# Optimization experiments

Hardware: AMD Instinct MI355X
Metric: run time of the kernel (lower is better)

Reference implementation:

```python
import jax, jax.numpy as jnp
import numpy as np

EPS = 1e-5

def _rms(x, w):
    # RMSNorm over last dim (head_dim), affine weight w
    v = jnp.mean(jnp.square(x), axis=-1, keepdims=True)
    return x * jax.lax.rsqrt(v + EPS) * w

def _rope(x, cos, sin):
    # x: [B, N, H, D]; cos/sin: [N, D] (interleaved-pair convention)
    xr = x.reshape(*x.shape[:-1], -1, 2)
    rot = jnp.stack([-xr[..., 1], xr[..., 0]], axis=-1).reshape(x.shape)
    return x * cos[None, :, None, :] + rot * sin[None, :, None, :]

def _rope_tables(n, d):
    pos = np.arange(n, dtype=np.float32)
    freqs = 1.0 / (10000.0 ** (np.arange(0, d, 2, dtype=np.float32) / d))
    ang = pos[:, None] * freqs[None, :]          # [n, d/2]
    ang = np.repeat(ang, 2, axis=1)              # [n, d] interleaved pairs
    return jnp.asarray(np.cos(ang)), jnp.asarray(np.sin(ang))

def setup_inputs() -> dict:
    key = jax.random.key(0)
    ks = jax.random.split(key, 6)
    B, N1, N2, C, H, D = 2, 1536, 512, 1024, 16, 64
    cos1, sin1 = _rope_tables(N1, D)
    cos2, sin2 = _rope_tables(N2, D)
    s = 0.02
    return dict(
        seq_len=N1,
        x=jax.random.normal(ks[0], (B, N1, C), jnp.float32),
        y=jax.random.normal(ks[1], (B, N2, C), jnp.float32),
        cos1=cos1, sin1=sin1, cos2=cos2, sin2=sin2,
        W_qkv_xs=jax.random.normal(ks[2], (3 * C, C), jnp.float32) * s,
        W_qkv_au=jax.random.normal(ks[3], (3 * C, C), jnp.float32) * s,
        xs_q_w=jnp.ones((D,), jnp.float32), xs_k_w=jnp.ones((D,), jnp.float32),
        au_q_w=jnp.ones((D,), jnp.float32), au_k_w=jnp.ones((D,), jnp.float32),
        W_xs_proj=jax.random.normal(ks[4], (C, C), jnp.float32) * s,
        b_xs_proj=jnp.zeros((C,), jnp.float32),
        W_au_proj=jax.random.normal(ks[5], (C, C), jnp.float32) * s,
        b_au_proj=jnp.zeros((C,), jnp.float32),
    )

def reference(seq_len, x, y, cos1, sin1, cos2, sin2,
              W_qkv_xs, W_qkv_au, xs_q_w, xs_k_w, au_q_w, au_k_w,
              W_xs_proj, b_xs_proj, W_au_proj, b_au_proj):
    B, N1, C = x.shape
    N2 = y.shape[1]
    D = xs_q_w.shape[0]
    H = C // D
    scale = D ** -0.5

    # visual stream: QKV -> per-head RMSNorm -> RoPE
    xq, xk, xv = jnp.split(x @ W_qkv_xs.T, 3, axis=-1)          # each [B,N1,C]
    xq = _rms(xq.reshape(B, N1, H, D), xs_q_w)
    xk = _rms(xk.reshape(B, N1, H, D), xs_k_w)
    xv = xv.reshape(B, N1, H, D).transpose(0, 2, 1, 3)           # [B,H,N1,D]
    xq = _rope(xq, cos1, sin1).transpose(0, 2, 1, 3)             # [B,H,N1,D]
    xk = _rope(xk, cos1, sin1).transpose(0, 2, 1, 3)

    # audio stream: QKV -> per-head RMSNorm -> RoPE
    aq, ak, av = jnp.split(y @ W_qkv_au.T, 3, axis=-1)
    aq = _rms(aq.reshape(B, N2, H, D), au_q_w)
    ak = _rms(ak.reshape(B, N2, H, D), au_k_w)
    av = av.reshape(B, N2, H, D).transpose(0, 2, 1, 3)           # [B,H,N2,D]
    aq = _rope(aq, cos2, sin2).transpose(0, 2, 1, 3)             # [B,H,N2,D]
    ak = _rope(ak, cos2, sin2).transpose(0, 2, 1, 3)

    # joint attention over concatenated sequence
    q = jnp.concatenate([xq, aq], axis=2)                        # [B,H,N1+N2,D]
    k = jnp.concatenate([xk, ak], axis=2)
    v = jnp.concatenate([xv, av], axis=2)
    attn = jax.nn.softmax(jnp.einsum('bhqd,bhkd->bhqk', q * scale, k), axis=-1)
    o = jnp.einsum('bhqk,bhkd->bhqd', attn, v)
    o = o.transpose(0, 2, 1, 3).reshape(B, N1 + N2, C)

    xs = o[:, :N1] @ W_xs_proj.T + b_xs_proj
    au = o[:, N1:] @ W_au_proj.T + b_au_proj
    return xs, au
```

## Files before the change

### kernel.cpp

```cpp
#include <hip/hip_runtime.h>
#include <hip/hip_bf16.h>

typedef __bf16 bf16_t;
typedef bf16_t bf16x4_t __attribute__((ext_vector_type(4)));
typedef bf16_t bf16x8_t __attribute__((ext_vector_type(8)));
typedef float f32x4_t __attribute__((ext_vector_type(4)));
typedef float f32x16_t __attribute__((ext_vector_type(16)));

constexpr int kB = 2, kN1 = 1536, kN2 = 512, kN = 2048, kC = 1024, kH = 16, kD = 64;
constexpr int BK = 64, LDT = 72;

__device__ inline uint32_t pack2bf(float a, float b) {
  union { bf16_t h[2]; uint32_t u; } t;
  t.h[0] = (bf16_t)a; t.h[1] = (bf16_t)b;
  return t.u;
}
__device__ inline void pl32_swap(uint32_t& a, uint32_t& b) {
  asm volatile("v_permlane32_swap_b32 %0, %1" : "+v"(a), "+v"(b));
}
__device__ __forceinline__ void gl16(const bf16_t* g, bf16_t* l) {
  __builtin_amdgcn_global_load_lds(
      (const __attribute__((address_space(1))) unsigned int*)g,
      (__attribute__((address_space(3))) unsigned int*)l, 16, 0, 0);
}

__global__ __launch_bounds__(256)
void cvt_bf16(const float* __restrict__ x, const float* __restrict__ y,
              const float* __restrict__ wqx, const float* __restrict__ wqa,
              const float* __restrict__ wpx, const float* __restrict__ wpa,
              bf16_t* __restrict__ Xb, bf16_t* __restrict__ Wq, bf16_t* __restrict__ Wp)
{
  const int bid = blockIdx.x;
  const float* src; bf16_t* dst; size_t off;
  if (bid < 192)      { src = x;   dst = Xb;           off = (size_t)bid * 16384; }
  else if (bid < 256) { src = y;   dst = Xb + 3145728; off = (size_t)(bid - 192) * 16384; }
  else if (bid < 448) { src = wqx; dst = Wq;           off = (size_t)(bid - 256) * 16384; }
  else if (bid < 640) { src = wqa; dst = Wq + 3145728; off = (size_t)(bid - 448) * 16384; }
  else if (bid < 704) { src = wpx; dst = Wp;           off = (size_t)(bid - 640) * 16384; }
  else                { src = wpa; dst = Wp + 1048576; off = (size_t)(bid - 704) * 16384; }
  src += off; dst += off;
  const int t = threadIdx.x;
  #pragma unroll
  for (int i = 0; i < 16; ++i) {
    const int e = (t + i * 256) * 4;
    f32x4_t v = *(const f32x4_t*)(src + e);
    bf16x4_t o;
    #pragma unroll
    for (int j = 0; j < 4; ++j) o[j] = (bf16_t)v[j];
    *(bf16x4_t*)(dst + e) = o;
  }
}

__global__ __launch_bounds__(256, 2)
void qkv_gemm(const bf16_t* __restrict__ Xb, const bf16_t* __restrict__ Wq,
              const float* __restrict__ cos1, const float* __restrict__ sin1,
              const float* __restrict__ cos2, const float* __restrict__ sin2,
              const float* __restrict__ xs_qw, const float* __restrict__ xs_kw,
              const float* __restrict__ au_qw, const float* __restrict__ au_kw,
              bf16_t* __restrict__ Qb, bf16_t* __restrict__ Kb, bf16_t* __restrict__ Vt)
{
  __shared__ __align__(16) bf16_t smem[32768];
  const int tid = threadIdx.x, lane = tid & 63, w = tid >> 6;
  const int wr = w >> 1, wc = w & 1;
  const int bm = blockIdx.x, bn = blockIdx.y;
  const int l15 = lane & 15, l4 = (lane >> 4) & 3;
  const int K = kC;
  const bool is_xs = bm < 24;

  const bf16_t* Ag = Xb + (size_t)bm * 128 * K;
  const bf16_t* Bg = Wq + (is_xs ? (size_t)0 : (size_t)3072 * 1024) + (size_t)bn * 128 * K;

  const int srow_l = lane >> 3;
  const int scc = (((lane & 7) ^ ((lane >> 3) & 7)) << 3);

  auto stage = [&](int c, int kt) {
    const int k0 = kt * BK;
    bf16_t* Ab = smem + c * 8192;
    bf16_t* Bb = smem + 16384 + c * 8192;
    #pragma unroll
    for (int i = 0; i < 4; ++i) {
      const int row = w * 32 + i * 8 + srow_l;
      gl16(Ag + (size_t)row * K + k0 + scc, Ab + (w * 32 + i * 8) * 64);
      gl16(Bg + (size_t)row * K + k0 + scc, Bb + (w * 32 + i * 8) * 64);
    }
  };

  f32x4_t acc[4][4] = {};
  const int nk = K / BK;
  stage(0, 0);
  asm volatile("s_waitcnt vmcnt(0)" ::: "memory");
  __syncthreads();

  int cur = 0;
  for (int kt = 0; kt < nk; ++kt) {
    if (kt + 1 < nk) stage(cur ^ 1, kt + 1);
    const bf16_t* Ab = smem + cur * 8192;
    const bf16_t* Bb = smem + 16384 + cur * 8192;
    #pragma unroll
    for (int kk = 0; kk < 2; ++kk) {
      bf16x8_t a[4], b[4];
      #pragma unroll
      for (int m = 0; m < 4; ++m) {
        const int row = wr * 64 + m * 16 + l15;
        const int cc = (kk * 32 + l4 * 8) ^ ((row & 7) << 3);
        a[m] = *(const bf16x8_t*)&Ab[row * 64 + cc];
      }
      #pragma unroll
      for (int n = 0; n < 4; ++n) {
        const int row = wc * 64 + n * 16 + l15;
        const int cc = (kk * 32 + l4 * 8) ^ ((row & 7) << 3);
        b[n] = *(const bf16x8_t*)&Bb[row * 64 + cc];
      }
      #pragma unroll
      for (int m = 0; m < 4; ++m)
        #pragma unroll
        for (int n = 0; n < 4; ++n)
          acc[m][n] = __builtin_amdgcn_mfma_f32_16x16x32_bf16(a[m], b[n], acc[m][n], 0, 0, 0);
    }
    asm volatile("s_waitcnt vmcnt(0)" ::: "memory");
    __syncthreads();
    cur ^= 1;
  }

  const int sec = bn >> 3;
  const int grow0 = bm * 128;
  int b, n0, seq_off; const float* cT; const float* sT;
  if (is_xs) { b = grow0 / 1536; n0 = grow0 - b * 1536; seq_off = 0; cT = cos1; sT = sin1; }
  else { const int g2 = grow0 - 3072; b = g2 >> 9; n0 = g2 & 511; seq_off = 1536; cT = cos2; sT = sin2; }
  const int h = (bn & 7) * 2 + wc;

  if (sec < 2) {
    const float* wsel = is_xs ? (sec == 0 ? xs_qw : xs_kw) : (sec == 0 ? au_qw : au_kw);
    float wv[4];
    #pragma unroll
    for (int n = 0; n < 4; ++n) wv[n] = wsel[n * 16 + l15];
    bf16_t* Out = (sec == 0 ? Qb : Kb) + (((size_t)b * kH + h) * kN + seq_off + n0) * kD;
    const float qscale = (sec == 0) ? 0.125f * 1.44269504088896f : 1.0f;
    #pragma unroll
    for (int m = 0; m < 4; ++m)
      #pragma unroll
      for (int r = 0; r < 4; ++r) {
        const int rl = wr * 64 + m * 16 + l4 * 4 + r;
        float ss = 0.0f;
        #pragma unroll
        for (int n = 0; n < 4; ++n) ss += acc[m][n][r] * acc[m][n][r];
        ss += __shfl_xor(ss, 1); ss += __shfl_xor(ss, 2);
        ss += __shfl_xor(ss, 4); ss += __shfl_xor(ss, 8);
        const float rinv = rsqrtf(ss * (1.0f / 64.0f) + 1e-5f);
        const int nrow = n0 + rl;
        #pragma unroll
        for (int n = 0; n < 4; ++n) {
          const int dd = n * 16 + l15;
          const float xn = acc[m][n][r] * rinv * wv[n];
          const float partner = __shfl_xor(xn, 1);
          if (!(l15 & 1)) {
            const float c = cT[(size_t)nrow * 64 + dd];
            const float s = sT[(size_t)nrow * 64 + dd];
            const float ve = (xn * c - partner * s) * qscale;
            const float vo = (partner * c + xn * s) * qscale;
            *(uint32_t*)&Out[(size_t)rl * kD + dd] = pack2bf(ve, vo);
          }
        }
      }
  } else {
    bf16_t* Lt = smem;
    #pragma unroll
    for (int m = 0; m < 4; ++m)
      #pragma unroll
      for (int n = 0; n < 4; ++n) {
        const int col = wc * 64 + n * 16 + l15;
        #pragma unroll
        for (int j = 0; j < 2; ++j) {
          const int row = wr * 64 + m * 16 + l4 * 4 + j * 2;
          *(uint32_t*)&Lt[col * 136 + row] = pack2bf(acc[m][n][j * 2], acc[m][n][j * 2 + 1]);
        }
      }
    __syncthreads();
    const int seg = tid >> 1, half = tid & 1;
    const int hl = seg >> 6, dd = seg & 63;
    bf16_t* Vo = Vt + (((size_t)b * kH + (bn & 7) * 2 + hl) * kD + dd) * kN
                 + seq_off + n0 + half * 64;
    #pragma unroll
    for (int jj = 0; jj < 8; ++jj)
      *(bf16x8_t*)&Vo[jj * 8] = *(const bf16x8_t*)&Lt[seg * 136 + half * 64 + jj * 8];
  }
}

__global__ __launch_bounds__(256, 2)
void proj_gemm(const bf16_t* __restrict__ Ob, const bf16_t* __restrict__ Wp,
               const float* __restrict__ bxs, const float* __restrict__ bau,
               float* __restrict__ out)
{
  __shared__ __align__(16) bf16_t smem[32768];
  const int tid = threadIdx.x, lane = tid & 63, w = tid >> 6;
  const int wr = w >> 1, wc = w & 1;
  const int bm = blockIdx.x, bn = blockIdx.y;
  const int l15 = lane & 15, l4 = (lane >> 4) & 3;
  const int K = kC, N = kC;

  const int grow = bm * 128;
  const int b = grow >> 11, n0r = grow & 2047;
  const bf16_t* Bg; const float* bias; float* Cg;
  if (n0r < kN1) { Bg = Wp; bias = bxs; Cg = out + ((size_t)b * kN1 + n0r) * kC; }
  else { Bg = Wp + (size_t)1024 * 1024; bias = bau;
         Cg = out + (size_t)kB * kN1 * kC + ((size_t)b * kN2 + (n0r - kN1)) * kC; }
  Bg += (size_t)bn * 128 * K;
  const bf16_t* Ag = Ob + (size_t)grow * K;

  const int srow_l = lane >> 3;
  const int scc = (((lane & 7) ^ ((lane >> 3) & 7)) << 3);

  auto stage = [&](int c, int kt) {
    const int k0 = kt * BK;
    bf16_t* Ab = smem + c * 8192;
    bf16_t* Bb = smem + 16384 + c * 8192;
    #pragma unroll
    for (int i = 0; i < 4; ++i) {
      const int row = w * 32 + i * 8 + srow_l;
      gl16(Ag + (size_t)row * K + k0 + scc, Ab + (w * 32 + i * 8) * 64);
      gl16(Bg + (size_t)row * K + k0 + scc, Bb + (w * 32 + i * 8) * 64);
    }
  };

  f32x4_t acc[4][4] = {};
  const int nk = K / BK;
  stage(0, 0);
  asm volatile("s_waitcnt vmcnt(0)" ::: "memory");
  __syncthreads();

  int cur = 0;
  for (int kt = 0; kt < nk; ++kt) {
    if (kt + 1 < nk) stage(cur ^ 1, kt + 1);
    const bf16_t* Ab = smem + cur * 8192;
    const bf16_t* Bb = smem + 16384 + cur * 8192;
    #pragma unroll
    for (int kk = 0; kk < 2; ++kk) {
      bf16x8_t a[4], bfr[4];
      #pragma unroll
      for (int m = 0; m < 4; ++m) {
        const int row = wr * 64 + m * 16 + l15;
        const int cc = (kk * 32 + l4 * 8) ^ ((row & 7) << 3);
        a[m] = *(const bf16x8_t*)&Ab[row * 64 + cc];
      }
      #pragma unroll
      for (int n = 0; n < 4; ++n) {
        const int row = wc * 64 + n * 16 + l15;
        const int cc = (kk * 32 + l4 * 8) ^ ((row & 7) << 3);
        bfr[n] = *(const bf16x8_t*)&Bb[row * 64 + cc];
      }
      #pragma unroll
      for (int m = 0; m < 4; ++m)
        #pragma unroll
        for (int n = 0; n < 4; ++n)
          acc[m][n] = __builtin_amdgcn_mfma_f32_16x16x32_bf16(a[m], bfr[n], acc[m][n], 0, 0, 0);
    }
    asm volatile("s_waitcnt vmcnt(0)" ::: "memory");
    __syncthreads();
    cur ^= 1;
  }

  float bv[4];
  #pragma unroll
  for (int n = 0; n < 4; ++n) bv[n] = bias[bn * 128 + wc * 64 + n * 16 + l15];
  #pragma unroll
  for (int m = 0; m < 4; ++m)
    #pragma unroll
    for (int n = 0; n < 4; ++n) {
      const int col = bn * 128 + wc * 64 + n * 16 + l15;
      #pragma unroll
      for (int r = 0; r < 4; ++r) {
        const int row = wr * 64 + m * 16 + l4 * 4 + r;
        Cg[(size_t)row * N + col] = acc[m][n][r] + bv[n];
      }
    }
}

__global__ __launch_bounds__(512, 2)
void flash_attn(const bf16_t* __restrict__ Q, const bf16_t* __restrict__ K,
                const bf16_t* __restrict__ Vt, bf16_t* __restrict__ O)
{
  __shared__ __align__(16) bf16_t smem[18432];
  const int tid = threadIdx.x, lane = tid & 63, w = tid >> 6;
  const int l31 = lane & 31, hi8 = ((lane >> 5) << 3), hi4 = ((lane >> 5) << 2);
  const int qt = blockIdx.x, h = blockIdx.y, b = blockIdx.z;
  const size_t headoff = ((size_t)(b * kH + h)) * kN * kD;
  const bf16_t* Kg = K + headoff;
  const bf16_t* Vg = Vt + headoff;

  bf16x8_t qf[4];
  {
    const bf16_t* Qg = Q + headoff + (size_t)(qt * 256 + w * 32 + l31) * kD + hi8;
    #pragma unroll
    for (int ks = 0; ks < 4; ++ks) qf[ks] = *(const bf16x8_t*)(Qg + ks * 16);
  }
  bf16x8_t onesv;
  #pragma unroll
  for (int j = 0; j < 8; ++j) onesv[j] = (bf16_t)1.0f;

  const int srow = tid >> 3, sc = (tid & 7) * 8;
  bf16x8_t kreg = *(const bf16x8_t*)(Kg + srow * kD + sc);
  bf16x8_t vreg = *(const bf16x8_t*)(Vg + (size_t)srow * kN + sc);

  f32x16_t oA0 = {}, oA1 = {}, accl = {};

  for (int kt = 0; kt < kN / 64; ++kt) {
    const int cur = kt & 1;
    bf16_t* Kc = smem + cur * 4608;
    bf16_t* Vc = smem + 9216 + cur * 4608;
    *(bf16x8_t*)&Kc[srow * LDT + sc] = kreg;
    *(bf16x8_t*)&Vc[srow * LDT + sc] = vreg;
    if (kt + 1 < kN / 64) {
      kreg = *(const bf16x8_t*)(Kg + (size_t)(kt + 1) * 64 * kD + srow * kD + sc);
      vreg = *(const bf16x8_t*)(Vg + (size_t)srow * kN + (kt + 1) * 64 + sc);
    }
    __syncthreads();

    f32x16_t s0 = {}, s1 = {};
    #pragma unroll
    for (int ks = 0; ks < 4; ++ks) {
      bf16x8_t k0 = *(const bf16x8_t*)&Kc[l31 * LDT + ks * 16 + hi8];
      bf16x8_t k1 = *(const bf16x8_t*)&Kc[(32 + l31) * LDT + ks * 16 + hi8];
      s0 = __builtin_amdgcn_mfma_f32_32x32x16_bf16(k0, qf[ks], s0, 0, 0, 0);
      s1 = __builtin_amdgcn_mfma_f32_32x32x16_bf16(k1, qf[ks], s1, 0, 0, 0);
    }

    #pragma unroll
    for (int i = 0; i < 16; ++i) {
      s0[i] = __builtin_amdgcn_exp2f(s0[i]);
      s1[i] = __builtin_amdgcn_exp2f(s1[i]);
    }

    union PW { uint32_t wd[4]; bf16x8_t v; } pf[4];
    #pragma unroll
    for (int o = 0; o < 2; ++o) {
      #pragma unroll
      for (int hh = 0; hh < 2; ++hh) {
        const int h8 = hh * 8, ks = o * 2 + hh;
        float p0, p1, p2, p3, p4, p5, p6, p7;
        if (o == 0) {
          p0 = s0[h8+0]; p1 = s0[h8+1]; p2 = s0[h8+2]; p3 = s0[h8+3];
          p4 = s0[h8+4]; p5 = s0[h8+5]; p6 = s0[h8+6]; p7 = s0[h8+7];
        } else {
          p0 = s1[h8+0]; p1 = s1[h8+1]; p2 = s1[h8+2]; p3 = s1[h8+3];
          p4 = s1[h8+4]; p5 = s1[h8+5]; p6 = s1[h8+6]; p7 = s1[h8+7];
        }
        uint32_t xw  = pack2bf(p0, p1), x2 = pack2bf(p2, p3);
        uint32_t yw  = pack2bf(p4, p5), y2 = pack2bf(p6, p7);
        pl32_swap(xw, yw);
        pl32_swap(x2, y2);
        pf[ks].wd[0] = xw; pf[ks].wd[1] = x2; pf[ks].wd[2] = yw; pf[ks].wd[3] = y2;
      }
    }

    #pragma unroll
    for (int ks = 0; ks < 4; ++ks) {
      bf16x8_t v0 = *(const bf16x8_t*)&Vc[l31 * LDT + ks * 16 + hi8];
      bf16x8_t v1 = *(const bf16x8_t*)&Vc[(32 + l31) * LDT + ks * 16 + hi8];
      oA0 = __builtin_amdgcn_mfma_f32_32x32x16_bf16(v0, pf[ks].v, oA0, 0, 0, 0);
      oA1 = __builtin_amdgcn_mfma_f32_32x32x16_bf16(v1, pf[ks].v, oA1, 0, 0, 0);
      accl = __builtin_amdgcn_mfma_f32_32x32x16_bf16(onesv, pf[ks].v, accl, 0, 0, 0);
    }
  }

  __syncthreads();
  bf16_t* Ow = smem + w * 2304;
  const float inv = 1.0f / accl[0];
  #pragma unroll
  for (int db = 0; db < 2; ++db) {
    f32x16_t o = db ? oA1 : oA0;
    #pragma unroll
    for (int rp = 0; rp < 8; ++rp) {
      const int d = db * 32 + ((rp & 1) << 1) + ((rp >> 1) << 3) + hi4;
      *(uint32_t*)&Ow[l31 * LDT + d] = pack2bf(o[2 * rp] * inv, o[2 * rp + 1] * inv);
    }
  }
  const int rq = lane >> 1, half = lane & 1;
  bf16x8_t r0 = *(const bf16x8_t*)&Ow[rq * LDT + half * 32];
  bf16x8_t r1 = *(const bf16x8_t*)&Ow[rq * LDT + half * 32 + 8];
  bf16x8_t r2 = *(const bf16x8_t*)&Ow[rq * LDT + half * 32 + 16];
  bf16x8_t r3 = *(const bf16x8_t*)&Ow[rq * LDT + half * 32 + 24];
  bf16_t* Og = O + ((size_t)b * kN + qt * 256 + w * 32 + rq) * kC + h * kD + half * 32;
  *(bf16x8_t*)&Og[0]  = r0;
  *(bf16x8_t*)&Og[8]  = r1;
  *(bf16x8_t*)&Og[16] = r2;
  *(bf16x8_t*)&Og[24] = r3;
}

extern "C" void kernel_launch(void* const* d_in, const int* in_sizes, int n_in,
                              void* d_out, int out_size, void* d_ws, size_t ws_size,
                              hipStream_t stream) {
  const float* x    = (const float*)d_in[1];
  const float* y    = (const float*)d_in[2];
  const float* cos1 = (const float*)d_in[3];
  const float* sin1 = (const float*)d_in[4];
  const float* cos2 = (const float*)d_in[5];
  const float* sin2 = (const float*)d_in[6];
  const float* Wqkv_xs = (const float*)d_in[7];
  const float* Wqkv_au = (const float*)d_in[8];
  const float* xs_q_w  = (const float*)d_in[9];
  const float* xs_k_w  = (const float*)d_in[10];
  const float* au_q_w  = (const float*)d_in[11];
  const float* au_k_w  = (const float*)d_in[12];
  const float* Wxs = (const float*)d_in[13];
  const float* bxs = (const float*)d_in[14];
  const float* Wau = (const float*)d_in[15];
  const float* bau = (const float*)d_in[16];
  float* out = (float*)d_out;

  char* ws = (char*)d_ws;
  bf16_t* Xb = (bf16_t*)(ws);
  bf16_t* Wq = (bf16_t*)(ws + 8388608);
  bf16_t* Wp = (bf16_t*)(ws + 20971520);
  bf16_t* Qb = (bf16_t*)(ws + 25165824);
  bf16_t* Kb = (bf16_t*)(ws + 33554432);
  bf16_t* Vt = (bf16_t*)(ws + 41943040);
  bf16_t* Ob = (bf16_t*)(ws + 50331648);

  cvt_bf16<<<dim3(768), dim3(256), 0, stream>>>(x, y, Wqkv_xs, Wqkv_au, Wxs, Wau, Xb, Wq, Wp);
  qkv_gemm<<<dim3(32, 24), dim3(256), 0, stream>>>(Xb, Wq, cos1, sin1, cos2, sin2,
      xs_q_w, xs_k_w, au_q_w, au_k_w, Qb, Kb, Vt);
  flash_attn<<<dim3(kN / 256, kH, kB), dim3(512), 0, stream>>>(Qb, Kb, Vt, Ob);
  proj_gemm<<<dim3(32, 8), dim3(256), 0, stream>>>(Ob, Wp, bxs, bau, out);
}
```

Before: 129.5 us.

## Enlarge QKV GEMM tile to 256x256 with 512 threads and XCD-aware block remap

The QKV projection GEMM moves from 128x128 tiles with 4 waves to 256x256 tiles with 8 waves, each wave computing 128x64. The grid becomes a 1D launch of 192 blocks remapped so neighbouring tiles land on the same XCD. The goal is more operand reuse per LDS load and less global traffic, and to cut partial-wave scheduling across the CUs. The K-loop sync is also relaxed with a partial vmcnt wait, and the V transpose epilogue now uses a per-wave swizzled LDS buffer. In exchange it uses 128KB of LDS and more accumulator registers, and 192 blocks leave some of the 256 CUs idle.

```diff
diff --git a/kernel.cpp b/kernel.cpp
--- a/kernel.cpp
+++ b/kernel.cpp
@@ -51,7 +51,7 @@
   }
 }
 
-__global__ __launch_bounds__(256, 2)
+__global__ __launch_bounds__(512, 2)
 void qkv_gemm(const bf16_t* __restrict__ Xb, const bf16_t* __restrict__ Wq,
               const float* __restrict__ cos1, const float* __restrict__ sin1,
               const float* __restrict__ cos2, const float* __restrict__ sin2,
@@ -59,52 +59,53 @@
               const float* __restrict__ au_qw, const float* __restrict__ au_kw,
               bf16_t* __restrict__ Qb, bf16_t* __restrict__ Kb, bf16_t* __restrict__ Vt)
 {
-  __shared__ __align__(16) bf16_t smem[32768];
+  __shared__ __align__(16) bf16_t smem[65536];
   const int tid = threadIdx.x, lane = tid & 63, w = tid >> 6;
-  const int wr = w >> 1, wc = w & 1;
-  const int bm = blockIdx.x, bn = blockIdx.y;
+  const int wr = w >> 2, wc = w & 3;
   const int l15 = lane & 15, l4 = (lane >> 4) & 3;
   const int K = kC;
-  const bool is_xs = bm < 24;
-
-  const bf16_t* Ag = Xb + (size_t)bm * 128 * K;
-  const bf16_t* Bg = Wq + (is_xs ? (size_t)0 : (size_t)3072 * 1024) + (size_t)bn * 128 * K;
-
-  const int srow_l = lane >> 3;
+
+  const int lin = blockIdx.x;
+  const int wgid = (lin & 7) * 24 + (lin >> 3);
+  const int bm = wgid / 12, bn = wgid % 12;
+  const bool is_xs = bm < 12;
+
+  const bf16_t* Ag = Xb + (size_t)bm * 256 * K;
+  const bf16_t* Bg = Wq + (is_xs ? (size_t)0 : (size_t)3072 * 1024) + (size_t)bn * 256 * K;
+
   const int scc = (((lane & 7) ^ ((lane >> 3) & 7)) << 3);
 
   auto stage = [&](int c, int kt) {
     const int k0 = kt * BK;
-    bf16_t* Ab = smem + c * 8192;
-    bf16_t* Bb = smem + 16384 + c * 8192;
+    bf16_t* Ab = smem + c * 16384;
+    bf16_t* Bb = smem + 32768 + c * 16384;
     #pragma unroll
     for (int i = 0; i < 4; ++i) {
-      const int row = w * 32 + i * 8 + srow_l;
+      const int row = w * 32 + i * 8 + (lane >> 3);
       gl16(Ag + (size_t)row * K + k0 + scc, Ab + (w * 32 + i * 8) * 64);
       gl16(Bg + (size_t)row * K + k0 + scc, Bb + (w * 32 + i * 8) * 64);
     }
   };
 
-  f32x4_t acc[4][4] = {};
+  f32x4_t acc[8][4] = {};
   const int nk = K / BK;
   stage(0, 0);
-  asm volatile("s_waitcnt vmcnt(0)" ::: "memory");
-  __syncthreads();
 
   int cur = 0;
   for (int kt = 0; kt < nk; ++kt) {
-    if (kt + 1 < nk) stage(cur ^ 1, kt + 1);
-    const bf16_t* Ab = smem + cur * 8192;
-    const bf16_t* Bb = smem + 16384 + cur * 8192;
+    if (kt + 1 < nk) {
+      stage(cur ^ 1, kt + 1);
+      asm volatile("s_waitcnt vmcnt(8)" ::: "memory");
+    } else {
+      asm volatile("s_waitcnt vmcnt(0)" ::: "memory");
+    }
+    __syncthreads();
+
+    const bf16_t* Ab = smem + cur * 16384;
+    const bf16_t* Bb = smem + 32768 + cur * 16384;
     #pragma unroll
     for (int kk = 0; kk < 2; ++kk) {
-      bf16x8_t a[4], b[4];
-      #pragma unroll
-      for (int m = 0; m < 4; ++m) {
-        const int row = wr * 64 + m * 16 + l15;
-        const int cc = (kk * 32 + l4 * 8) ^ ((row & 7) << 3);
-        a[m] = *(const bf16x8_t*)&Ab[row * 64 + cc];
-      }
+      bf16x8_t b[4];
       #pragma unroll
       for (int n = 0; n < 4; ++n) {
         const int row = wc * 64 + n * 16 + l15;
@@ -112,22 +113,25 @@
         b[n] = *(const bf16x8_t*)&Bb[row * 64 + cc];
       }
       #pragma unroll
-      for (int m = 0; m < 4; ++m)
+      for (int m = 0; m < 8; ++m) {
+        const int row = wr * 128 + m * 16 + l15;
+        const int cc = (kk * 32 + l4 * 8) ^ ((row & 7) << 3);
+        bf16x8_t a = *(const bf16x8_t*)&Ab[row * 64 + cc];
         #pragma unroll
         for (int n = 0; n < 4; ++n)
-          acc[m][n] = __builtin_amdgcn_mfma_f32_16x16x32_bf16(a[m], b[n], acc[m][n], 0, 0, 0);
-    }
-    asm volatile("s_waitcnt vmcnt(0)" ::: "memory");
+          acc[m][n] = __builtin_amdgcn_mfma_f32_16x16x32_bf16(a, b[n], acc[m][n], 0, 0, 0);
+      }
+    }
     __syncthreads();
     cur ^= 1;
   }
 
-  const int sec = bn >> 3;
-  const int grow0 = bm * 128;
+  const int sec = bn >> 2;
+  const int grow0 = bm * 256;
   int b, n0, seq_off; const float* cT; const float* sT;
   if (is_xs) { b = grow0 / 1536; n0 = grow0 - b * 1536; seq_off = 0; cT = cos1; sT = sin1; }
   else { const int g2 = grow0 - 3072; b = g2 >> 9; n0 = g2 & 511; seq_off = 1536; cT = cos2; sT = sin2; }
-  const int h = (bn & 7) * 2 + wc;
+  const int h = (bn & 3) * 4 + wc;
 
   if (sec < 2) {
     const float* wsel = is_xs ? (sec == 0 ? xs_qw : xs_kw) : (sec == 0 ? au_qw : au_kw);
@@ -137,10 +141,10 @@
     bf16_t* Out = (sec == 0 ? Qb : Kb) + (((size_t)b * kH + h) * kN + seq_off + n0) * kD;
     const float qscale = (sec == 0) ? 0.125f * 1.44269504088896f : 1.0f;
     #pragma unroll
-    for (int m = 0; m < 4; ++m)
+    for (int m = 0; m < 8; ++m)
       #pragma unroll
       for (int r = 0; r < 4; ++r) {
-        const int rl = wr * 64 + m * 16 + l4 * 4 + r;
+        const int rl = wr * 128 + m * 16 + l4 * 4 + r;
         float ss = 0.0f;
         #pragma unroll
         for (int n = 0; n < 4; ++n) ss += acc[m][n][r] * acc[m][n][r];
@@ -163,26 +167,26 @@
         }
       }
   } else {
-    bf16_t* Lt = smem;
-    #pragma unroll
-    for (int m = 0; m < 4; ++m)
+    bf16_t* Lt = smem + w * 8192;
+    #pragma unroll
+    for (int m = 0; m < 8; ++m)
       #pragma unroll
       for (int n = 0; n < 4; ++n) {
-        const int col = wc * 64 + n * 16 + l15;
+        const int dd = n * 16 + l15;
+        const int sw = (dd & 7) << 4;
         #pragma unroll
         for (int j = 0; j < 2; ++j) {
-          const int row = wr * 64 + m * 16 + l4 * 4 + j * 2;
-          *(uint32_t*)&Lt[col * 136 + row] = pack2bf(acc[m][n][j * 2], acc[m][n][j * 2 + 1]);
+          const int rll = m * 16 + l4 * 4 + j * 2;
+          *(uint32_t*)&Lt[dd * 128 + (rll ^ sw)] = pack2bf(acc[m][n][j * 2], acc[m][n][j * 2 + 1]);
         }
       }
     __syncthreads();
-    const int seg = tid >> 1, half = tid & 1;
-    const int hl = seg >> 6, dd = seg & 63;
-    bf16_t* Vo = Vt + (((size_t)b * kH + (bn & 7) * 2 + hl) * kD + dd) * kN
-                 + seq_off + n0 + half * 64;
-    #pragma unroll
-    for (int jj = 0; jj < 8; ++jj)
-      *(bf16x8_t*)&Vo[jj * 8] = *(const bf16x8_t*)&Lt[seg * 136 + half * 64 + jj * 8];
+    const int dd = lane;
+    const int sw = (dd & 7) << 4;
+    bf16_t* Vo = Vt + (((size_t)b * kH + h) * kD + dd) * kN + seq_off + n0 + wr * 128;
+    #pragma unroll
+    for (int jj = 0; jj < 16; ++jj)
+      *(bf16x8_t*)&Vo[jj * 8] = *(const bf16x8_t*)&Lt[dd * 128 + ((jj * 8) ^ sw)];
   }
 }
 
@@ -417,7 +421,7 @@
   bf16_t* Ob = (bf16_t*)(ws + 50331648);
 
   cvt_bf16<<<dim3(768), dim3(256), 0, stream>>>(x, y, Wqkv_xs, Wqkv_au, Wxs, Wau, Xb, Wq, Wp);
-  qkv_gemm<<<dim3(32, 24), dim3(256), 0, stream>>>(Xb, Wq, cos1, sin1, cos2, sin2,
+  qkv_gemm<<<dim3(192), dim3(512), 0, stream>>>(Xb, Wq, cos1, sin1, cos2, sin2,
       xs_q_w, xs_k_w, au_q_w, au_k_w, Qb, Kb, Vt);
   flash_attn<<<dim3(kN / 256, kH, kB), dim3(512), 0, stream>>>(Qb, Kb, Vt, Ob);
   proj_gemm<<<dim3(32, 8), dim3(256), 0, stream>>>(Ob, Wp, bxs, bau, out);
```

Result: slower. 148.6 us (+14.7%).
